# Optimization experiments

Measured on AMD Instinct MI355X. Metric: run time of the kernel, lower is better.

## Reference

```python
import jax, jax.numpy as jnp
import numpy as np

HIDDEN = 1024
HEADS = 16
HEAD = HIDDEN // HEADS


def setup_inputs() -> dict:
    key = jax.random.key(0)
    ks = jax.random.split(key, 6)
    B, T = 2, 2048
    x = jax.random.normal(ks[0], (B, T, HIDDEN), dtype=jnp.float32)
    mask = jnp.ones((T, T), dtype=jnp.float32)
    s = 1.0 / np.sqrt(HIDDEN)
    Wqkv = jax.random.normal(ks[1], (HIDDEN, 3 * HIDDEN), dtype=jnp.float32) * s
    bqkv = jnp.zeros((3 * HIDDEN,), dtype=jnp.float32)
    Wproj = jax.random.normal(ks[2], (HIDDEN, HIDDEN), dtype=jnp.float32) * s
    bproj = jnp.zeros((HIDDEN,), dtype=jnp.float32)
    return {"x": x, "mask": mask, "Wqkv": Wqkv, "bqkv": bqkv,
            "Wproj": Wproj, "bproj": bproj}


def reference(x, mask, Wqkv, bqkv, Wproj, bproj):
    B, T, C = x.shape
    qkv = x @ Wqkv + bqkv                      # [B,T,3C]
    q, k, v = jnp.split(qkv, 3, axis=-1)
    def heads(t):                              # [B,T,C] -> [B,H,T,D]
        return t.reshape(B, T, HEADS, HEAD).transpose(0, 2, 1, 3)
    q, k, v = heads(q), heads(k), heads(v)
    scores = jnp.einsum('bhqd,bhkd->bhqk', q, k) / np.sqrt(HEAD)
    scores = jnp.where(mask == 0, -jnp.inf, scores)
    attn = jax.nn.softmax(scores, axis=-1)
    out = jnp.einsum('bhqk,bhkd->bhqd', attn, v)
    out = out.transpose(0, 2, 1, 3).reshape(B, T, C)
    return out @ Wproj + bproj
```

## Files before the change

### kernel.cpp

```cpp
#include <hip/hip_runtime.h>
#include <stdint.h>

#define HID 1024
#define NH 16
#define HD 64
#define BATCH 2
#define SEQ 2048
#define MR (BATCH*SEQ)
#define NQKV (3*HID)

typedef __attribute__((ext_vector_type(8))) _Float16 h16x8;
typedef __attribute__((ext_vector_type(4))) _Float16 h16x4;
typedef __attribute__((ext_vector_type(2))) __fp16 fp16x2;
typedef __attribute__((ext_vector_type(8))) unsigned short u16x8;
typedef __attribute__((ext_vector_type(4))) float f32x4;

#if __has_builtin(__builtin_amdgcn_exp2f)
#define EXP2(x) __builtin_amdgcn_exp2f(x)
#else
#define EXP2(x) exp2f(x)
#endif

static __device__ __forceinline__ unsigned short f2h(float f) {
  union { _Float16 h; unsigned short u; } v; v.h = (_Float16)f; return v.u;
}
static __device__ __forceinline__ unsigned pk2(float a, float b) {
  union { fp16x2 h; unsigned u; } v;
  v.h = __builtin_amdgcn_cvt_pkrtz(a, b);
  return v.u;
}

typedef const __attribute__((address_space(1))) unsigned int glb_u32;
typedef __attribute__((address_space(3))) unsigned int lds_u32;
static __device__ __forceinline__ void cp16(const void* g, void* l) {
  __builtin_amdgcn_global_load_lds((glb_u32*)g, (lds_u32*)l, 16, 0, 0);
}

#define QSCL (0.125f * 1.44269504f)

__global__ __launch_bounds__(256) void k_prep(const float4* __restrict__ x4,
                                              const float* __restrict__ mask,
                                              const float* __restrict__ Wqkv,
                                              const float* __restrict__ Wproj,
                                              u16x8* __restrict__ xh8,
                                              unsigned short* __restrict__ WqT,
                                              unsigned short* __restrict__ WpT,
                                              unsigned long long* __restrict__ mb) {
  __shared__ float tile[64 * 65];
  int blk = blockIdx.x, tid = threadIdx.x;
  if (blk < 2048) {
    int i = blk * 256 + tid;
    float4 a = x4[2 * i], b = x4[2 * i + 1];
    u16x8 h;
    h[0] = f2h(a.x); h[1] = f2h(a.y); h[2] = f2h(a.z); h[3] = f2h(a.w);
    h[4] = f2h(b.x); h[5] = f2h(b.y); h[6] = f2h(b.z); h[7] = f2h(b.w);
    xh8[i] = h;
  } else if (blk < 3072) {
    const float* src; unsigned short* dst; int C, bx, by;
    if (blk < 2816) { src = Wqkv;  dst = WqT; C = NQKV; int b2 = blk - 2048; bx = b2 % 48; by = b2 / 48; }
    else            { src = Wproj; dst = WpT; C = HID;  int b2 = blk - 2816; bx = b2 & 15; by = b2 >> 4; }
    int col0 = bx * 64, row0 = by * 64;
    #pragma unroll
    for (int p = 0; p < 4; p++) {
      int idx = tid + p * 256;
      int r = idx >> 4, c4 = idx & 15;
      float4 v = *(const float4*)&src[(size_t)(row0 + r) * C + col0 + c4 * 4];
      int base = r * 65 + c4 * 4;
      tile[base] = v.x; tile[base + 1] = v.y; tile[base + 2] = v.z; tile[base + 3] = v.w;
    }
    __syncthreads();
    #pragma unroll
    for (int p = 0; p < 2; p++) {
      int idx = tid + p * 256;
      int oc = idx >> 3, ch = idx & 7;
      u16x8 w;
      #pragma unroll
      for (int j = 0; j < 8; j++) w[j] = f2h(tile[(ch * 8 + j) * 65 + oc]);
      *(u16x8*)&dst[(size_t)(col0 + oc) * HID + row0 + ch * 8] = w;
    }
  } else {
    int gw0 = (blk - 3072) * 64 + (tid >> 6) * 16;
    int lane = tid & 63;
    #pragma unroll
    for (int j = 0; j < 16; j++) {
      float v = mask[(size_t)(gw0 + j) * 64 + lane];
      unsigned long long b = __ballot(v != 0.f);
      if (lane == 0) mb[gw0 + j] = b;
    }
  }
}

__global__ __launch_bounds__(256) void k_gemm_qkv(const unsigned short* __restrict__ A,
                                                  const unsigned short* __restrict__ Bt,
                                                  const float* __restrict__ bias,
                                                  unsigned short* __restrict__ Qp,
                                                  unsigned short* __restrict__ Kp,
                                                  unsigned short* __restrict__ Vt) {
  int tid = threadIdx.x;
  int wave = tid >> 6, lane = tid & 63, quad = lane >> 4, l16 = lane & 15;
  int wm = wave >> 1, wn = wave & 1;
  int x7 = l16 & 7;
  int blk = blockIdx.x;
  int orig = (blk & 7) * 96 + (blk >> 3);
  int m0 = (orig / 24) * 128, n0 = (orig % 24) * 128;
  __shared__ __align__(16) unsigned short smem[32768];
  unsigned short* Lb = smem;

  auto stage = [&](unsigned short* buf, int k0) {
    #pragma unroll
    for (int i = 0; i < 4; i++) {
      int c = tid + i * 256;
      int r = c >> 3, sc = ((c ^ r) & 7) << 3;
      cp16(&A[(size_t)(m0 + r) * HID + k0 + sc], &buf[c << 3]);
      cp16(&Bt[(size_t)(n0 + r) * HID + k0 + sc], &buf[8192 + (c << 3)]);
    }
  };
  stage(smem, 0);
  f32x4 acc[4][4] = {};
  __syncthreads();
  for (int kt = 0; kt < 16; kt++) {
    unsigned short* cb = smem + ((kt & 1) << 14);
    if (kt < 15) stage(smem + (((kt + 1) & 1) << 14), (kt + 1) * 64);
    #pragma unroll
    for (int kc = 0; kc < 2; kc++) {
      h16x8 af[4], bf[4];
      #pragma unroll
      for (int i = 0; i < 4; i++) {
        af[i] = *(const h16x8*)&cb[(wm * 64 + i * 16 + l16) * 64 + (((kc * 4 + quad) ^ x7) << 3)];
        bf[i] = *(const h16x8*)&cb[8192 + (wn * 64 + i * 16 + l16) * 64 + (((kc * 4 + quad) ^ x7) << 3)];
      }
      __builtin_amdgcn_s_setprio(1);
      #pragma unroll
      for (int i = 0; i < 4; i++)
        #pragma unroll
        for (int j = 0; j < 4; j++)
          acc[i][j] = __builtin_amdgcn_mfma_f32_16x16x32_f16(af[i], bf[j], acc[i][j], 0, 0, 0);
      __builtin_amdgcn_s_setprio(0);
    }
    asm volatile("s_waitcnt vmcnt(0)" ::: "memory");
    __builtin_amdgcn_s_barrier();
    __builtin_amdgcn_sched_barrier(0);
  }
  int which = n0 >> 10;
  int hbase = (n0 & 1023) >> 6;
  if (which == 2) {
    #pragma unroll
    for (int j = 0; j < 4; j++) {
      int nl = wn * 64 + j * 16 + l16;
      float bv = bias[n0 + nl];
      #pragma unroll
      for (int i = 0; i < 4; i++) {
        int ml = wm * 64 + i * 16 + quad * 4;
        uint2 tt;
        tt.x = pk2(acc[i][j][0] + bv, acc[i][j][1] + bv);
        tt.y = pk2(acc[i][j][2] + bv, acc[i][j][3] + bv);
        *(uint2*)&Lb[nl * 136 + ml] = tt;
      }
    }
  } else {
    float scl = (which == 0) ? QSCL : 1.0f;
    #pragma unroll
    for (int j = 0; j < 4; j++) {
      int nl = wn * 64 + j * 16 + l16;
      float bv = bias[n0 + nl];
      #pragma unroll
      for (int i = 0; i < 4; i++)
        #pragma unroll
        for (int r = 0; r < 4; r++) {
          int ml = wm * 64 + i * 16 + quad * 4 + r;
          Lb[ml * 136 + nl] = f2h((acc[i][j][r] + bv) * scl);
        }
    }
  }
  __syncthreads();
  int b = m0 >> 11, tb = m0 & 2047;
  if (which == 2) {
    #pragma unroll
    for (int p = 0; p < 8; p++) {
      int c = tid + p * 256;
      int rr = c >> 4, cc = c & 15;
      int h = hbase + (rr >> 6), d = rr & 63;
      u16x8 vv = *(const u16x8*)&Lb[rr * 136 + cc * 8];
      *(u16x8*)&Vt[(size_t)(b * NH + h) * (SEQ * HD) + (size_t)d * SEQ + tb + cc * 8] = vv;
    }
  } else {
    unsigned short* dst = (which == 0) ? Qp : Kp;
    #pragma unroll
    for (int p = 0; p < 8; p++) {
      int c = tid + p * 256;
      int rr = c >> 4, cc = c & 15;
      int h = hbase + (cc >> 3), d0 = (cc & 7) << 3;
      u16x8 vv = *(const u16x8*)&Lb[rr * 136 + cc * 8];
      *(u16x8*)&dst[(size_t)(b * NH + h) * (SEQ * HD) + (size_t)(tb + rr) * HD + d0] = vv;
    }
  }
}

__global__ __launch_bounds__(256) void k_attn(const unsigned short* __restrict__ Qp,
                                              const unsigned short* __restrict__ Kp,
                                              const unsigned short* __restrict__ Vt,
                                              const unsigned long long* __restrict__ mb,
                                              unsigned short* __restrict__ AO) {
  int tid = threadIdx.x, wave = tid >> 6, lane = tid & 63, quad = lane >> 4, l16 = lane & 15;
  int lin = blockIdx.x + 16 * blockIdx.y;
  int orig = (lin & 7) * 64 + (lin >> 3);
  int bh = orig >> 4, qbase = (orig & 15) * 128;
  const unsigned short* Qg = Qp + (size_t)bh * (SEQ * HD);
  const unsigned short* Kg = Kp + (size_t)bh * (SEQ * HD);
  const unsigned short* Vg = Vt + (size_t)bh * (SEQ * HD);
  __shared__ __align__(16) unsigned short smem[24576];
  unsigned short* Qs = smem;
  unsigned short* Os = smem;

  #pragma unroll
  for (int i = 0; i < 4; i++) {
    int c = tid + i * 256;
    int row = c >> 3, sc = ((c ^ row) & 7) << 3;
    cp16(&Qg[(size_t)(qbase + row) * HD + sc], &Qs[c << 3]);
  }
  #pragma unroll
  for (int i = 0; i < 2; i++) {
    int c = tid + i * 256;
    int row = c >> 3, sc = ((c ^ row) & 7) << 3;
    cp16(&Kg[(size_t)row * HD + sc], &smem[8192 + (c << 3)]);
    cp16(&Vg[(size_t)row * SEQ + sc], &smem[12288 + (c << 3)]);
  }
  int q0 = qbase + wave * 32 + l16;
  const unsigned long long* mrow0 = mb + (size_t)q0 * 32;
  const unsigned long long* mrow1 = mb + (size_t)(q0 + 16) * 32;
  f32x4 acc_o[2][4] = {};
  f32x4 acc_l[2] = {};
  int x7 = l16 & 7;

  h16x4 vone4;
  #pragma unroll
  for (int j = 0; j < 4; j++) vone4[j] = (_Float16)1.0f;

  __syncthreads();
  h16x8 bq[2][2];
  #pragma unroll
  for (int s = 0; s < 2; s++)
    #pragma unroll
    for (int kk = 0; kk < 2; kk++)
      bq[s][kk] = *(const h16x8*)&Qs[(wave * 32 + s * 16 + l16) * 64 + (((kk * 4 + quad) ^ x7) << 3)];

  for (int kt = 0; kt < 32; kt++) {
    unsigned short* cb = smem + 8192 + ((kt & 1) << 13);
    if (kt < 31) {
      unsigned short* nb = smem + 8192 + (((kt + 1) & 1) << 13);
      int kb2 = (kt + 1) * 64;
      #pragma unroll
      for (int i = 0; i < 2; i++) {
        int c = tid + i * 256;
        int row = c >> 3, sc = ((c ^ row) & 7) << 3;
        cp16(&Kg[(size_t)(kb2 + row) * HD + sc], &nb[c << 3]);
        cp16(&Vg[(size_t)row * SEQ + kb2 + sc], &nb[4096 + (c << 3)]);
      }
    }
    unsigned long long w0 = mrow0[kt], w1 = mrow1[kt];
    h16x8 ka[4][2];
    #pragma unroll
    for (int nt = 0; nt < 4; nt++)
      #pragma unroll
      for (int kk = 0; kk < 2; kk++)
        ka[nt][kk] = *(const h16x8*)&cb[(nt * 16 + l16) * 64 + (((kk * 4 + quad) ^ x7) << 3)];
    f32x4 s0[4] = {}, s1[4] = {};
    __builtin_amdgcn_s_setprio(1);
    #pragma unroll
    for (int nt = 0; nt < 4; nt++)
      #pragma unroll
      for (int kk = 0; kk < 2; kk++) {
        s0[nt] = __builtin_amdgcn_mfma_f32_16x16x32_f16(ka[nt][kk], bq[0][kk], s0[nt], 0, 0, 0);
        s1[nt] = __builtin_amdgcn_mfma_f32_16x16x32_f16(ka[nt][kk], bq[1][kk], s1[nt], 0, 0, 0);
      }
    __builtin_amdgcn_s_setprio(0);
    h16x4 va16[4][4];
    #pragma unroll
    for (int nt = 0; nt < 4; nt++)
      #pragma unroll
      for (int seg = 0; seg < 4; seg++)
        va16[nt][seg] = *(const h16x4*)&cb[4096 + (nt * 16 + l16) * 64 +
                                           (((seg * 2 + (quad >> 1)) ^ x7) << 3) +
                                           ((quad & 1) << 2)];
    if (!__all((w0 & w1) == ~0ULL)) {
      #pragma unroll
      for (int nt = 0; nt < 4; nt++)
        #pragma unroll
        for (int r = 0; r < 4; r++) {
          int bit = nt * 16 + quad * 4 + r;
          if (!((w0 >> bit) & 1ULL)) s0[nt][r] = -100.f;
          if (!((w1 >> bit) & 1ULL)) s1[nt][r] = -100.f;
        }
    }
    #pragma unroll
    for (int nt = 0; nt < 4; nt++)
      #pragma unroll
      for (int r = 0; r < 4; r++) {
        s0[nt][r] = EXP2(s0[nt][r]);
        s1[nt][r] = EXP2(s1[nt][r]);
      }
    auto pv = [&](const f32x4 (&s)[4], f32x4 (&ao)[4], f32x4 &al) {
      #pragma unroll
      for (int seg = 0; seg < 4; seg++) {
        union { h16x4 h; unsigned u[2]; } pb;
        pb.u[0] = pk2(s[seg][0], s[seg][1]);
        pb.u[1] = pk2(s[seg][2], s[seg][3]);
        al = __builtin_amdgcn_mfma_f32_16x16x16f16(vone4, pb.h, al, 0, 0, 0);
        #pragma unroll
        for (int nt = 0; nt < 4; nt++)
          ao[nt] = __builtin_amdgcn_mfma_f32_16x16x16f16(va16[nt][seg], pb.h, ao[nt], 0, 0, 0);
      }
    };
    __builtin_amdgcn_s_setprio(1);
    pv(s0, acc_o[0], acc_l[0]);
    pv(s1, acc_o[1], acc_l[1]);
    __builtin_amdgcn_s_setprio(0);
    asm volatile("s_waitcnt vmcnt(0)" ::: "memory");
    __builtin_amdgcn_s_barrier();
    __builtin_amdgcn_sched_barrier(0);
  }
  float rl0 = 1.0f / acc_l[0][0];
  float rl1 = 1.0f / acc_l[1][0];
  #pragma unroll
  for (int nt = 0; nt < 4; nt++) {
    uint2 t;
    t.x = (unsigned)f2h(acc_o[0][nt][0] * rl0) | ((unsigned)f2h(acc_o[0][nt][1] * rl0) << 16);
    t.y = (unsigned)f2h(acc_o[0][nt][2] * rl0) | ((unsigned)f2h(acc_o[0][nt][3] * rl0) << 16);
    *(uint2*)&Os[(wave * 32 + l16) * 72 + nt * 16 + quad * 4] = t;
    uint2 u;
    u.x = (unsigned)f2h(acc_o[1][nt][0] * rl1) | ((unsigned)f2h(acc_o[1][nt][1] * rl1) << 16);
    u.y = (unsigned)f2h(acc_o[1][nt][2] * rl1) | ((unsigned)f2h(acc_o[1][nt][3] * rl1) << 16);
    *(uint2*)&Os[(wave * 32 + 16 + l16) * 72 + nt * 16 + quad * 4] = u;
  }
  __syncthreads();
  int b = bh >> 4, h = bh & 15;
  #pragma unroll
  for (int i = 0; i < 4; i++) {
    int c = tid + i * 256;
    int row = c >> 3, co = (c & 7) << 3;
    u16x8 vv = *(const u16x8*)&Os[row * 72 + co];
    *(u16x8*)&AO[(size_t)(b * SEQ + qbase + row) * HID + h * HD + co] = vv;
  }
}

__global__ __launch_bounds__(256) void k_gemm_proj(const unsigned short* __restrict__ A,
                                                   const unsigned short* __restrict__ Bt,
                                                   const float* __restrict__ bias,
                                                   float* __restrict__ out) {
  int tid = threadIdx.x;
  int wave = tid >> 6, lane = tid & 63, quad = lane >> 4, l16 = lane & 15;
  int wm = wave >> 1, wn = wave & 1;
  int x7 = l16 & 7;
  int lin = blockIdx.x + 16 * blockIdx.y;
  int orig = (lin & 7) * 64 + (lin >> 3);
  int m0 = (orig >> 4) * 128, n0 = (orig & 15) * 64;
  __shared__ __align__(16) unsigned short smem[24576];
  float* Lf = (float*)smem;

  auto stage = [&](unsigned short* buf, int k0) {
    #pragma unroll
    for (int i = 0; i < 4; i++) {
      int c = tid + i * 256;
      int r = c >> 3, sc = ((c ^ r) & 7) << 3;
      cp16(&A[(size_t)(m0 + r) * HID + k0 + sc], &buf[c << 3]);
    }
    #pragma unroll
    for (int i = 0; i < 2; i++) {
      int c = tid + i * 256;
      int r = c >> 3, sc = ((c ^ r) & 7) << 3;
      cp16(&Bt[(size_t)(n0 + r) * HID + k0 + sc], &buf[8192 + (c << 3)]);
    }
  };
  stage(smem, 0);
  f32x4 acc[4][2] = {};
  __syncthreads();
  for (int kt = 0; kt < 16; kt++) {
    unsigned short* cb = smem + (kt & 1) * 12288;
    if (kt < 15) stage(smem + ((kt + 1) & 1) * 12288, (kt + 1) * 64);
    #pragma unroll
    for (int kc = 0; kc < 2; kc++) {
      h16x8 af[4], bf[2];
      #pragma unroll
      for (int i = 0; i < 4; i++)
        af[i] = *(const h16x8*)&cb[(wm * 64 + i * 16 + l16) * 64 + (((kc * 4 + quad) ^ x7) << 3)];
      #pragma unroll
      for (int j = 0; j < 2; j++)
        bf[j] = *(const h16x8*)&cb[8192 + (wn * 32 + j * 16 + l16) * 64 + (((kc * 4 + quad) ^ x7) << 3)];
      __builtin_amdgcn_s_setprio(1);
      #pragma unroll
      for (int i = 0; i < 4; i++)
        #pragma unroll
        for (int j = 0; j < 2; j++)
          acc[i][j] = __builtin_amdgcn_mfma_f32_16x16x32_f16(af[i], bf[j], acc[i][j], 0, 0, 0);
      __builtin_amdgcn_s_setprio(0);
    }
    asm volatile("s_waitcnt vmcnt(0)" ::: "memory");
    __builtin_amdgcn_s_barrier();
    __builtin_amdgcn_sched_barrier(0);
  }
  #pragma unroll
  for (int j = 0; j < 2; j++) {
    int nl = wn * 32 + j * 16 + l16;
    float bv = bias[n0 + nl];
    #pragma unroll
    for (int i = 0; i < 4; i++)
      #pragma unroll
      for (int r = 0; r < 4; r++) {
        int ml = wm * 64 + i * 16 + quad * 4 + r;
        Lf[ml * 68 + nl] = acc[i][j][r] + bv;
      }
  }
  __syncthreads();
  #pragma unroll
  for (int p = 0; p < 8; p++) {
    int c = tid + p * 256;
    int rr = c >> 4, cc = c & 15;
    float4 vv = *(const float4*)&Lf[rr * 68 + cc * 4];
    *(float4*)&out[(size_t)(m0 + rr) * HID + n0 + cc * 4] = vv;
  }
}

extern "C" void kernel_launch(void* const* d_in, const int* in_sizes, int n_in,
                              void* d_out, int out_size, void* d_ws, size_t ws_size,
                              hipStream_t stream) {
  const float* x     = (const float*)d_in[0];
  const float* mask  = (const float*)d_in[1];
  const float* Wqkv  = (const float*)d_in[2];
  const float* bqkv  = (const float*)d_in[3];
  const float* Wproj = (const float*)d_in[4];
  const float* bproj = (const float*)d_in[5];
  float* out = (float*)d_out;

  uint8_t* ws = (uint8_t*)d_ws;
  size_t off = 0;
  auto alloc = [&](size_t bytes) -> void* {
    void* p = (void*)(ws + off);
    off += (bytes + 255) & ~(size_t)255;
    return p;
  };
  unsigned short* xh   = (unsigned short*)alloc((size_t)MR * HID * 2);
  unsigned short* WqT  = (unsigned short*)alloc((size_t)NQKV * HID * 2);
  unsigned short* WpT  = (unsigned short*)alloc((size_t)HID * HID * 2);
  unsigned short* Qp   = (unsigned short*)alloc((size_t)BATCH * NH * SEQ * HD * 2);
  unsigned short* Kp   = (unsigned short*)alloc((size_t)BATCH * NH * SEQ * HD * 2);
  unsigned short* Vtp  = (unsigned short*)alloc((size_t)BATCH * NH * SEQ * HD * 2);
  unsigned short* AO   = (unsigned short*)alloc((size_t)MR * HID * 2);
  unsigned long long* mb = (unsigned long long*)alloc((size_t)SEQ * (SEQ / 64) * 8);

  k_prep<<<4096, 256, 0, stream>>>((const float4*)x, mask, Wqkv, Wproj,
                                   (u16x8*)xh, WqT, WpT, mb);
  k_gemm_qkv<<<768, 256, 0, stream>>>(xh, WqT, bqkv, Qp, Kp, Vtp);
  k_attn<<<dim3(SEQ / 128, BATCH * NH), 256, 0, stream>>>(Qp, Kp, Vtp, mb, AO);
  k_gemm_proj<<<dim3(HID / 64, MR / 128), 256, 0, stream>>>(AO, WpT, bproj, out);
}
```

Baseline: 201.3 us.

## Enlarge QKV GEMM tile to 256x128 with 512 threads, single-buffered

The QKV projection GEMM now uses 512-thread blocks computing 256x128 output tiles, halving the grid to 384 blocks so each B tile is reused across twice as many rows. To fit shared memory, the double-buffered async prefetch is replaced by a single buffer with barriers before and after each load. The epilogue is split into two halves that reuse the same staging buffer. Dropping the prefetch overlap exposes global-load latency on every k-step and adds synchronisation, and the smaller grid may underfill the GPU's compute units.

Result: slower. 215.0 us (+6.8%).

```diff
diff --git a/kernel.cpp b/kernel.cpp
--- a/kernel.cpp
+++ b/kernel.cpp
@@ -90,7 +90,7 @@
   }
 }
 
-__global__ __launch_bounds__(256) void k_gemm_qkv(const unsigned short* __restrict__ A,
+__global__ __launch_bounds__(512) void k_gemm_qkv(const unsigned short* __restrict__ A,
                                                   const unsigned short* __restrict__ Bt,
                                                   const float* __restrict__ bias,
                                                   unsigned short* __restrict__ Qp,
@@ -101,33 +101,36 @@
   int wm = wave >> 1, wn = wave & 1;
   int x7 = l16 & 7;
   int blk = blockIdx.x;
-  int orig = (blk & 7) * 96 + (blk >> 3);
-  int m0 = (orig / 24) * 128, n0 = (orig % 24) * 128;
-  __shared__ __align__(16) unsigned short smem[32768];
+  int orig = (blk & 7) * 48 + (blk >> 3);
+  int m0 = (orig / 24) * 256, n0 = (orig % 24) * 128;
+  __shared__ __align__(16) unsigned short smem[24576];
+  unsigned short* As = smem;
+  unsigned short* Bs = smem + 16384;
   unsigned short* Lb = smem;
 
-  auto stage = [&](unsigned short* buf, int k0) {
+  f32x4 acc[4][4] = {};
+  for (int k0 = 0; k0 < HID; k0 += 64) {
+    __syncthreads();
     #pragma unroll
     for (int i = 0; i < 4; i++) {
-      int c = tid + i * 256;
+      int c = tid + i * 512;
       int r = c >> 3, sc = ((c ^ r) & 7) << 3;
-      cp16(&A[(size_t)(m0 + r) * HID + k0 + sc], &buf[c << 3]);
-      cp16(&Bt[(size_t)(n0 + r) * HID + k0 + sc], &buf[8192 + (c << 3)]);
-    }
-  };
-  stage(smem, 0);
-  f32x4 acc[4][4] = {};
-  __syncthreads();
-  for (int kt = 0; kt < 16; kt++) {
-    unsigned short* cb = smem + ((kt & 1) << 14);
-    if (kt < 15) stage(smem + (((kt + 1) & 1) << 14), (kt + 1) * 64);
+      cp16(&A[(size_t)(m0 + r) * HID + k0 + sc], &As[c << 3]);
+    }
+    #pragma unroll
+    for (int i = 0; i < 2; i++) {
+      int c = tid + i * 512;
+      int r = c >> 3, sc = ((c ^ r) & 7) << 3;
+      cp16(&Bt[(size_t)(n0 + r) * HID + k0 + sc], &Bs[c << 3]);
+    }
+    __syncthreads();
     #pragma unroll
     for (int kc = 0; kc < 2; kc++) {
       h16x8 af[4], bf[4];
       #pragma unroll
       for (int i = 0; i < 4; i++) {
-        af[i] = *(const h16x8*)&cb[(wm * 64 + i * 16 + l16) * 64 + (((kc * 4 + quad) ^ x7) << 3)];
-        bf[i] = *(const h16x8*)&cb[8192 + (wn * 64 + i * 16 + l16) * 64 + (((kc * 4 + quad) ^ x7) << 3)];
+        af[i] = *(const h16x8*)&As[(wm * 64 + i * 16 + l16) * 64 + (((kc * 4 + quad) ^ x7) << 3)];
+        bf[i] = *(const h16x8*)&Bs[(wn * 64 + i * 16 + l16) * 64 + (((kc * 4 + quad) ^ x7) << 3)];
       }
       __builtin_amdgcn_s_setprio(1);
       #pragma unroll
@@ -137,61 +140,65 @@
           acc[i][j] = __builtin_amdgcn_mfma_f32_16x16x32_f16(af[i], bf[j], acc[i][j], 0, 0, 0);
       __builtin_amdgcn_s_setprio(0);
     }
-    asm volatile("s_waitcnt vmcnt(0)" ::: "memory");
-    __builtin_amdgcn_s_barrier();
-    __builtin_amdgcn_sched_barrier(0);
   }
   int which = n0 >> 10;
   int hbase = (n0 & 1023) >> 6;
-  if (which == 2) {
-    #pragma unroll
-    for (int j = 0; j < 4; j++) {
-      int nl = wn * 64 + j * 16 + l16;
-      float bv = bias[n0 + nl];
-      #pragma unroll
-      for (int i = 0; i < 4; i++) {
-        int ml = wm * 64 + i * 16 + quad * 4;
-        uint2 tt;
-        tt.x = pk2(acc[i][j][0] + bv, acc[i][j][1] + bv);
-        tt.y = pk2(acc[i][j][2] + bv, acc[i][j][3] + bv);
-        *(uint2*)&Lb[nl * 136 + ml] = tt;
-      }
-    }
-  } else {
-    float scl = (which == 0) ? QSCL : 1.0f;
-    #pragma unroll
-    for (int j = 0; j < 4; j++) {
-      int nl = wn * 64 + j * 16 + l16;
-      float bv = bias[n0 + nl];
-      #pragma unroll
-      for (int i = 0; i < 4; i++)
-        #pragma unroll
-        for (int r = 0; r < 4; r++) {
-          int ml = wm * 64 + i * 16 + quad * 4 + r;
-          Lb[ml * 136 + nl] = f2h((acc[i][j][r] + bv) * scl);
+  int b = m0 >> 11, tb = m0 & 2047;
+  #pragma unroll
+  for (int half = 0; half < 2; half++) {
+    __syncthreads();
+    if ((wm >> 1) == half) {
+      int wml = wm & 1;
+      if (which == 2) {
+        #pragma unroll
+        for (int j = 0; j < 4; j++) {
+          int nl = wn * 64 + j * 16 + l16;
+          float bv = bias[n0 + nl];
+          #pragma unroll
+          for (int i = 0; i < 4; i++) {
+            int ml = wml * 64 + i * 16 + quad * 4;
+            uint2 tt;
+            tt.x = pk2(acc[i][j][0] + bv, acc[i][j][1] + bv);
+            tt.y = pk2(acc[i][j][2] + bv, acc[i][j][3] + bv);
+            *(uint2*)&Lb[nl * 136 + ml] = tt;
+          }
         }
-    }
-  }
-  __syncthreads();
-  int b = m0 >> 11, tb = m0 & 2047;
-  if (which == 2) {
-    #pragma unroll
-    for (int p = 0; p < 8; p++) {
-      int c = tid + p * 256;
-      int rr = c >> 4, cc = c & 15;
-      int h = hbase + (rr >> 6), d = rr & 63;
-      u16x8 vv = *(const u16x8*)&Lb[rr * 136 + cc * 8];
-      *(u16x8*)&Vt[(size_t)(b * NH + h) * (SEQ * HD) + (size_t)d * SEQ + tb + cc * 8] = vv;
-    }
-  } else {
-    unsigned short* dst = (which == 0) ? Qp : Kp;
-    #pragma unroll
-    for (int p = 0; p < 8; p++) {
-      int c = tid + p * 256;
-      int rr = c >> 4, cc = c & 15;
-      int h = hbase + (cc >> 3), d0 = (cc & 7) << 3;
-      u16x8 vv = *(const u16x8*)&Lb[rr * 136 + cc * 8];
-      *(u16x8*)&dst[(size_t)(b * NH + h) * (SEQ * HD) + (size_t)(tb + rr) * HD + d0] = vv;
+      } else {
+        float scl = (which == 0) ? QSCL : 1.0f;
+        #pragma unroll
+        for (int j = 0; j < 4; j++) {
+          int nl = wn * 64 + j * 16 + l16;
+          float bv = bias[n0 + nl];
+          #pragma unroll
+          for (int i = 0; i < 4; i++)
+            #pragma unroll
+            for (int r = 0; r < 4; r++) {
+              int ml = wml * 64 + i * 16 + quad * 4 + r;
+              Lb[ml * 136 + nl] = f2h((acc[i][j][r] + bv) * scl);
+            }
+        }
+      }
+    }
+    __syncthreads();
+    if (which == 2) {
+      #pragma unroll
+      for (int p = 0; p < 4; p++) {
+        int c = tid + p * 512;
+        int rr = c >> 4, cc = c & 15;
+        int h = hbase + (rr >> 6), d = rr & 63;
+        u16x8 vv = *(const u16x8*)&Lb[rr * 136 + cc * 8];
+        *(u16x8*)&Vt[(size_t)(b * NH + h) * (SEQ * HD) + (size_t)d * SEQ + tb + half * 128 + cc * 8] = vv;
+      }
+    } else {
+      unsigned short* dst = (which == 0) ? Qp : Kp;
+      #pragma unroll
+      for (int p = 0; p < 4; p++) {
+        int c = tid + p * 512;
+        int rr = c >> 4, cc = c & 15;
+        int h = hbase + (cc >> 3), d0 = (cc & 7) << 3;
+        u16x8 vv = *(const u16x8*)&Lb[rr * 136 + cc * 8];
+        *(u16x8*)&dst[(size_t)(b * NH + h) * (SEQ * HD) + (size_t)(tb + half * 128 + rr) * HD + d0] = vv;
+      }
     }
   }
 }
@@ -449,7 +456,7 @@
 
   k_prep<<<4096, 256, 0, stream>>>((const float4*)x, mask, Wqkv, Wproj,
                                    (u16x8*)xh, WqT, WpT, mb);
-  k_gemm_qkv<<<768, 256, 0, stream>>>(xh, WqT, bqkv, Qp, Kp, Vtp);
+  k_gemm_qkv<<<384, 512, 0, stream>>>(xh, WqT, bqkv, Qp, Kp, Vtp);
   k_attn<<<dim3(SEQ / 128, BATCH * NH), 256, 0, stream>>>(Qp, Kp, Vtp, mb, AO);
   k_gemm_proj<<<dim3(HID / 64, MR / 128), 256, 0, stream>>>(AO, WpT, bproj, out);
 }
```
